# Performance work log

Measured on AMD Instinct MI355X. Metric: run time of the kernel, lower is better.

The kernel has to match this reference:

```python
import jax, jax.numpy as jnp
import numpy as np

B, C, H, W = 16, 64, 128, 128


def setup_inputs() -> dict:
    key = jax.random.key(0)
    k1, k2, k3 = jax.random.split(key, 3)
    return {
        "template_map": jax.random.normal(k1, (B, C, H, W), dtype=jnp.float32),
        "roi_map": jax.random.normal(k2, (B, C, H, W), dtype=jnp.float32),
        "gamma": jnp.zeros((1,), dtype=jnp.float32),
        "omega": jnp.zeros((1,), dtype=jnp.float32),
        "conv_w": jax.random.normal(k3, (C, 2 * C), dtype=jnp.float32) * 0.05,
        "conv_b": jnp.zeros((C,), dtype=jnp.float32),
    }


def _chan_attn(x):
    # x: [B, C, H, W] -> attention over channels [B, C, C] and flat values [B, C, N]
    b, c, h, w = x.shape
    v = x.reshape(b, c, h * w)
    energy = jnp.einsum('bcn,bdn->bcd', v, v)  # [B, C, C]
    energy_new = jnp.max(energy, axis=-1, keepdims=True) - energy
    attn = jax.nn.softmax(energy_new, axis=-1)
    return attn, v


def reference(template_map, roi_map, gamma, omega, conv_w, conv_b):
    b, c, th, tw = template_map.shape
    _, _, rh, rw = roi_map.shape
    t_attn, t_v = _chan_attn(template_map)
    r_attn, r_v = _chan_attn(roi_map)
    # cross application: roi attention reweights template channels, and vice versa
    t_out = jnp.einsum('bcd,bdn->bcn', r_attn, t_v).reshape(b, c, th, tw)
    t_out = gamma * t_out + template_map
    r_out = jnp.einsum('bcd,bdn->bcn', t_attn, r_v).reshape(b, c, rh, rw)
    r_out = omega * r_out + roi_map
    fused = jnp.concatenate([t_out, r_out], axis=1)  # [B, 2C, H, W]
    # 1x1 conv == channel-mixing einsum
    out = jnp.einsum('bchw,oc->bohw', fused, conv_w) + conv_b[None, :, None, None]
    return out
```

## Files before the change

### kernel.cpp

```cpp
#include <hip/hip_runtime.h>

typedef __attribute__((ext_vector_type(8))) short short8;
typedef __attribute__((ext_vector_type(4))) float floatx4;
typedef unsigned int uint;
typedef unsigned short ushort;

#define BATCH 16
#define CH 64
#define NPIX 16384
#define TWOC 128

__device__ __forceinline__ ushort f2bf(float f) {
    uint u = __float_as_uint(f);
    u += 0x7FFFu + ((u >> 16) & 1u);
    return (ushort)(u >> 16);
}

__global__ __launch_bounds__(256) void gram_kernel(
    const float* __restrict__ tmap, const float* __restrict__ rmap,
    const float* __restrict__ gamma, const float* __restrict__ omega,
    float* __restrict__ G)
{
    const int map = blockIdx.y;
    const float mult = (map == 0) ? omega[0] : gamma[0];
    if (mult == 0.f) return;

    __shared__ float tile[64][68];
    const int chunk = blockIdx.x;
    const int b     = blockIdx.z;
    const float* x = (map == 0 ? tmap : rmap) + (size_t)b * CH * NPIX + chunk * 512;
    const int t  = threadIdx.x;
    const int ti = t >> 4;
    const int tj = t & 15;

    float acc[4][4];
#pragma unroll
    for (int i = 0; i < 4; ++i)
#pragma unroll
        for (int j = 0; j < 4; ++j) acc[i][j] = 0.f;

    for (int tt = 0; tt < 8; ++tt) {
        const int col0 = tt * 64;
#pragma unroll
        for (int k = 0; k < 16; ++k) {
            int e = t + 256 * k;
            int c = e >> 6, col = e & 63;
            tile[c][col] = x[(size_t)c * NPIX + col0 + col];
        }
        __syncthreads();
#pragma unroll 8
        for (int n = 0; n < 64; n += 2) {
            float2 av[4], bv[4];
#pragma unroll
            for (int i = 0; i < 4; ++i) av[i] = *(const float2*)&tile[ti + 16 * i][n];
#pragma unroll
            for (int j = 0; j < 4; ++j) bv[j] = *(const float2*)&tile[tj + 16 * j][n];
#pragma unroll
            for (int i = 0; i < 4; ++i)
#pragma unroll
                for (int j = 0; j < 4; ++j) {
                    acc[i][j] += av[i].x * bv[j].x;
                    acc[i][j] += av[i].y * bv[j].y;
                }
        }
        __syncthreads();
    }
    float* Gp = G + ((size_t)(b * 2 + map) << 12);
#pragma unroll
    for (int i = 0; i < 4; ++i)
#pragma unroll
        for (int j = 0; j < 4; ++j)
            atomicAdd(&Gp[(ti + 16 * i) * 64 + (tj + 16 * j)], acc[i][j]);
}

__global__ __launch_bounds__(128) void finalize_kernel(
    const float* __restrict__ G, const float* __restrict__ gamma,
    const float* __restrict__ omega, const float* __restrict__ conv_w,
    ushort* __restrict__ Mtf)
{
    __shared__ float attn[2][64][64];
    const int b = blockIdx.x;
    const int t = threadIdx.x;
    const float gam = gamma[0], om = omega[0];
    {
        const int map = t >> 6, i = t & 63;
        const float need = (map == 0) ? om : gam;
        if (need != 0.f) {
            const float* Grow = G + ((size_t)(b * 2 + map) << 12) + i * 64;
            float mn = Grow[0];
            for (int j = 1; j < 64; ++j) mn = fminf(mn, Grow[j]);
            float s = 0.f;
            for (int j = 0; j < 64; ++j) s += expf(mn - Grow[j]);
            const float inv = 1.f / s;
            for (int j = 0; j < 64; ++j) attn[map][i][j] = expf(mn - Grow[j]) * inv;
        }
    }
    __syncthreads();
    for (int idx = t; idx < 8192; idx += 128) {
        const int e     = idx & 7;
        const int l     = (idx >> 3) & 63;
        const int mi    = (idx >> 9) & 3;
        const int kstep = idx >> 11;
        const int row = mi * 16 + (l & 15);
        const int k   = kstep * 32 + (l >> 4) * 8 + e;
        const float* wrow = conv_w + row * TWOC;
        float v = wrow[k];
        if (k < 64) {
            if (gam != 0.f) {
                float dot = 0.f;
                for (int c = 0; c < 64; ++c) dot += wrow[c] * attn[1][c][k];
                v += gam * dot;
            }
        } else {
            const int d = k - 64;
            if (om != 0.f) {
                float dot = 0.f;
                for (int c = 0; c < 64; ++c) dot += wrow[64 + c] * attn[0][c][d];
                v += om * dot;
            }
        }
        Mtf[(size_t)b * 8192 + idx] = f2bf(v);
    }
}

__global__ __launch_bounds__(256, 3) void out_kernel(
    const float* __restrict__ tmap, const float* __restrict__ rmap,
    const ushort* __restrict__ Mtf, const float* __restrict__ conv_b,
    float* __restrict__ out)
{
    const int b   = blockIdx.y;
    const int t   = threadIdx.x;
    const int w   = t >> 6;
    const int l   = t & 63;
    const int lg  = l >> 4;
    const int lj  = l & 15;
    const int pxw = blockIdx.x * 256 + w * 64;

    const ushort* mbase = Mtf + (size_t)b * 8192;

    floatx4 acc[4][4];
#pragma unroll
    for (int mi = 0; mi < 4; ++mi)
#pragma unroll
        for (int nj = 0; nj < 4; ++nj) acc[mi][nj] = (floatx4){0.f, 0.f, 0.f, 0.f};

#pragma unroll
    for (int h = 0; h < 2; ++h) {
        const float* src = ((h == 0) ? tmap : rmap) + (size_t)b * CH * NPIX;
#pragma unroll
        for (int ks = 0; ks < 2; ++ks) {
            short8 a[4];
#pragma unroll
            for (int mi = 0; mi < 4; ++mi)
                a[mi] = *(const short8*)&mbase[((((h * 2 + ks) * 4 + mi) * 64) + l) * 8];

#pragma unroll
            for (int nj = 0; nj < 4; ++nj) {
                const float* cbase = src + (size_t)(ks * 32 + lg * 8) * NPIX
                                         + pxw + nj * 16 + lj;
                float v[8];
#pragma unroll
                for (int e = 0; e < 8; ++e) v[e] = cbase[(size_t)e * NPIX];
                short8 bb;
#pragma unroll
                for (int e = 0; e < 8; ++e) bb[e] = (short)f2bf(v[e]);
#pragma unroll
                for (int mi = 0; mi < 4; ++mi)
                    acc[mi][nj] = __builtin_amdgcn_mfma_f32_16x16x32_bf16(
                        a[mi], bb, acc[mi][nj], 0, 0, 0);
            }
        }
    }

#pragma unroll
    for (int mi = 0; mi < 4; ++mi) {
#pragma unroll
        for (int r = 0; r < 4; ++r) {
            const int och = mi * 16 + lg * 4 + r;
            const float bv = conv_b[och];
            float* orow = out + ((size_t)b * CH + och) * NPIX;
#pragma unroll
            for (int nj = 0; nj < 4; ++nj)
                orow[pxw + nj * 16 + lj] = acc[mi][nj][r] + bv;
        }
    }
}

extern "C" void kernel_launch(void* const* d_in, const int* in_sizes, int n_in,
                              void* d_out, int out_size, void* d_ws, size_t ws_size,
                              hipStream_t stream) {
    const float* tmap   = (const float*)d_in[0];
    const float* rmap   = (const float*)d_in[1];
    const float* gamma  = (const float*)d_in[2];
    const float* omega  = (const float*)d_in[3];
    const float* conv_w = (const float*)d_in[4];
    const float* conv_b = (const float*)d_in[5];
    float* out = (float*)d_out;

    float*  G   = (float*)d_ws;
    ushort* Mtf = (ushort*)((char*)d_ws + (size_t)BATCH * 2 * 4096 * sizeof(float));

    hipMemsetAsync(d_ws, 0, (size_t)BATCH * 2 * 4096 * sizeof(float), stream);

    gram_kernel<<<dim3(32, 2, BATCH), 256, 0, stream>>>(tmap, rmap, gamma, omega, G);
    finalize_kernel<<<dim3(BATCH), 128, 0, stream>>>(G, gamma, omega, conv_w, Mtf);
    out_kernel<<<dim3(64, BATCH), 256, 0, stream>>>(tmap, rmap, Mtf, conv_b, out);
}
```

Measured before the change: 53.52 us.

## Stage bf16 input tiles and weight matrix in LDS for out_kernel MFMA

out_kernel now copies the per-batch bf16 mixing matrix into shared memory and loads input channels as float4 vectors. Pairs of channels are packed to bf16 and written to a padded LDS tile, and the MFMA B operands are then gathered from that tile. This replaces the scalar strided global loads, one float per channel per lane, with wide coalesced loads. In exchange it adds LDS traffic and two barriers per chunk, and the occupancy hint rises from 3 to 4 blocks.

New measurement: 54.46 us. Within noise of the previous version (+1.8%).

```diff
diff --git a/kernel.cpp b/kernel.cpp
--- a/kernel.cpp
+++ b/kernel.cpp
@@ -9,11 +9,15 @@
 #define CH 64
 #define NPIX 16384
 #define TWOC 128
+#define XSTR 260
 
 __device__ __forceinline__ ushort f2bf(float f) {
     uint u = __float_as_uint(f);
     u += 0x7FFFu + ((u >> 16) & 1u);
     return (ushort)(u >> 16);
+}
+__device__ __forceinline__ uint pk2(float lo, float hi) {
+    return (uint)f2bf(lo) | ((uint)f2bf(hi) << 16);
 }
 
 __global__ __launch_bounds__(256) void gram_kernel(
@@ -123,20 +127,28 @@
     }
 }
 
-__global__ __launch_bounds__(256, 3) void out_kernel(
+__global__ __launch_bounds__(256, 4) void out_kernel(
     const float* __restrict__ tmap, const float* __restrict__ rmap,
     const ushort* __restrict__ Mtf, const float* __restrict__ conv_b,
     float* __restrict__ out)
 {
+    __shared__ __align__(16) ushort Ms[8192];
+    __shared__ __align__(16) uint   Xs[16 * XSTR];
+
     const int b   = blockIdx.y;
     const int t   = threadIdx.x;
     const int w   = t >> 6;
     const int l   = t & 63;
     const int lg  = l >> 4;
     const int lj  = l & 15;
-    const int pxw = blockIdx.x * 256 + w * 64;
-
-    const ushort* mbase = Mtf + (size_t)b * 8192;
+    const int px0 = blockIdx.x * 256;
+
+    {
+        const uint4* src = (const uint4*)(Mtf + (size_t)b * 8192);
+        uint4* dst = (uint4*)Ms;
+#pragma unroll
+        for (int i = 0; i < 4; ++i) dst[t + 256 * i] = src[t + 256 * i];
+    }
 
     floatx4 acc[4][4];
 #pragma unroll
@@ -144,34 +156,56 @@
 #pragma unroll
         for (int nj = 0; nj < 4; ++nj) acc[mi][nj] = (floatx4){0.f, 0.f, 0.f, 0.f};
 
-#pragma unroll
-    for (int h = 0; h < 2; ++h) {
-        const float* src = ((h == 0) ? tmap : rmap) + (size_t)b * CH * NPIX;
-#pragma unroll
-        for (int ks = 0; ks < 2; ++ks) {
-            short8 a[4];
+    const float* tb = tmap + (size_t)b * CH * NPIX + px0;
+    const float* rb = rmap + (size_t)b * CH * NPIX + px0;
+
+#pragma unroll
+    for (int c = 0; c < 4; ++c) {
+        const float* src = ((c < 2) ? tb : rb) + (size_t)((c & 1) * 32) * NPIX;
+
+        float4 r0[4], r1[4];
+#pragma unroll
+        for (int it = 0; it < 4; ++it) {
+            const int p = it * 4 + w;
+            r0[it] = *(const float4*)&src[(size_t)(2 * p) * NPIX + 4 * l];
+            r1[it] = *(const float4*)&src[(size_t)(2 * p + 1) * NPIX + 4 * l];
+        }
+        __syncthreads();
+
+#pragma unroll
+        for (int it = 0; it < 4; ++it) {
+            const int p = it * 4 + w;
+            uint4 o;
+            o.x = pk2(r0[it].x, r1[it].x);
+            o.y = pk2(r0[it].y, r1[it].y);
+            o.z = pk2(r0[it].z, r1[it].z);
+            o.w = pk2(r0[it].w, r1[it].w);
+            *(uint4*)&Xs[p * XSTR + 4 * l] = o;
+        }
+        __syncthreads();
+
+        short8 a[4];
+#pragma unroll
+        for (int mi = 0; mi < 4; ++mi)
+            a[mi] = *(const short8*)&Ms[((c * 4 + mi) * 64 + l) * 8];
+
+#pragma unroll
+        for (int nj = 0; nj < 4; ++nj) {
+            const int pxl = w * 64 + nj * 16 + lj;
+            uint4 bu;
+            bu.x = Xs[(4 * lg + 0) * XSTR + pxl];
+            bu.y = Xs[(4 * lg + 1) * XSTR + pxl];
+            bu.z = Xs[(4 * lg + 2) * XSTR + pxl];
+            bu.w = Xs[(4 * lg + 3) * XSTR + pxl];
+            const short8 bb = *(const short8*)&bu;
 #pragma unroll
             for (int mi = 0; mi < 4; ++mi)
-                a[mi] = *(const short8*)&mbase[((((h * 2 + ks) * 4 + mi) * 64) + l) * 8];
-
-#pragma unroll
-            for (int nj = 0; nj < 4; ++nj) {
-                const float* cbase = src + (size_t)(ks * 32 + lg * 8) * NPIX
-                                         + pxw + nj * 16 + lj;
-                float v[8];
-#pragma unroll
-                for (int e = 0; e < 8; ++e) v[e] = cbase[(size_t)e * NPIX];
-                short8 bb;
-#pragma unroll
-                for (int e = 0; e < 8; ++e) bb[e] = (short)f2bf(v[e]);
-#pragma unroll
-                for (int mi = 0; mi < 4; ++mi)
-                    acc[mi][nj] = __builtin_amdgcn_mfma_f32_16x16x32_bf16(
-                        a[mi], bb, acc[mi][nj], 0, 0, 0);
-            }
-        }
-    }
-
+                acc[mi][nj] = __builtin_amdgcn_mfma_f32_16x16x32_bf16(
+                    a[mi], bb, acc[mi][nj], 0, 0, 0);
+        }
+    }
+
+    const int pxw = px0 + w * 64;
 #pragma unroll
     for (int mi = 0; mi < 4; ++mi) {
 #pragma unroll
```

## Stage out_kernel inputs via global_load_lds and vectorize output stores through LDS

Applied to the files above, without the earlier changes.

out_kernel now loads each 32-channel x 256-pixel slab into shared memory with 16-byte direct global-to-LDS loads. Previously each lane issued strided scalar 4-byte loads. Results are staged back through LDS so the output is written with 16-byte vector stores instead of scalar ones, and the occupancy hint rises from 3 to 4 blocks per SIMD. The cost is 32 KB of LDS per block, extra barriers with no double buffering, and possible LDS bank conflicts on the transposed reads.

Result: slower. 68.53 us (+28.0%).

```diff
diff --git a/kernel.cpp b/kernel.cpp
--- a/kernel.cpp
+++ b/kernel.cpp
@@ -14,6 +14,15 @@
     uint u = __float_as_uint(f);
     u += 0x7FFFu + ((u >> 16) & 1u);
     return (ushort)(u >> 16);
+}
+__device__ __forceinline__ uint pk2(float lo, float hi) {
+    return (uint)f2bf(lo) | ((uint)f2bf(hi) << 16);
+}
+
+typedef const __attribute__((address_space(1))) void gas_void;
+typedef __attribute__((address_space(3))) void las_void;
+__device__ __forceinline__ void gload16(const void* g, void* l) {
+    __builtin_amdgcn_global_load_lds((gas_void*)g, (las_void*)l, 16, 0, 0);
 }
 
 __global__ __launch_bounds__(256) void gram_kernel(
@@ -123,20 +132,24 @@
     }
 }
 
-__global__ __launch_bounds__(256, 3) void out_kernel(
+__global__ __launch_bounds__(256, 4) void out_kernel(
     const float* __restrict__ tmap, const float* __restrict__ rmap,
     const ushort* __restrict__ Mtf, const float* __restrict__ conv_b,
     float* __restrict__ out)
 {
+    __shared__ __align__(16) uint Xs[32 * 256];
+
     const int b   = blockIdx.y;
     const int t   = threadIdx.x;
     const int w   = t >> 6;
     const int l   = t & 63;
     const int lg  = l >> 4;
     const int lj  = l & 15;
-    const int pxw = blockIdx.x * 256 + w * 64;
+    const int px0 = blockIdx.x * 256;
 
     const ushort* mbase = Mtf + (size_t)b * 8192;
+    const float*  tb = tmap + (size_t)b * CH * NPIX + px0;
+    const float*  rb = rmap + (size_t)b * CH * NPIX + px0;
 
     floatx4 acc[4][4];
 #pragma unroll
@@ -145,44 +158,68 @@
         for (int nj = 0; nj < 4; ++nj) acc[mi][nj] = (floatx4){0.f, 0.f, 0.f, 0.f};
 
 #pragma unroll
-    for (int h = 0; h < 2; ++h) {
-        const float* src = ((h == 0) ? tmap : rmap) + (size_t)b * CH * NPIX;
-#pragma unroll
-        for (int ks = 0; ks < 2; ++ks) {
-            short8 a[4];
+    for (int c = 0; c < 4; ++c) {
+        const float* src = ((c < 2) ? tb : rb) + (size_t)((c & 1) * 32) * NPIX;
+
+#pragma unroll
+        for (int i = 0; i < 8; ++i) {
+            const int row = i * 4 + w;
+            gload16(src + (size_t)row * NPIX + 4 * l, &Xs[row * 256]);
+        }
+
+        short8 a[4];
+#pragma unroll
+        for (int mi = 0; mi < 4; ++mi)
+            a[mi] = *(const short8*)&mbase[((c * 4 + mi) * 64 + l) * 8];
+
+        __syncthreads();
+
+#pragma unroll
+        for (int nj = 0; nj < 4; ++nj) {
+            const int pxl = w * 64 + nj * 16 + lj;
+            float v[8];
+#pragma unroll
+            for (int e = 0; e < 8; ++e)
+                v[e] = __uint_as_float(Xs[(8 * lg + e) * 256 + pxl]);
+            uint4 bu;
+            bu.x = pk2(v[0], v[1]);
+            bu.y = pk2(v[2], v[3]);
+            bu.z = pk2(v[4], v[5]);
+            bu.w = pk2(v[6], v[7]);
+            const short8 bb = *(const short8*)&bu;
 #pragma unroll
             for (int mi = 0; mi < 4; ++mi)
-                a[mi] = *(const short8*)&mbase[((((h * 2 + ks) * 4 + mi) * 64) + l) * 8];
-
-#pragma unroll
-            for (int nj = 0; nj < 4; ++nj) {
-                const float* cbase = src + (size_t)(ks * 32 + lg * 8) * NPIX
-                                         + pxw + nj * 16 + lj;
-                float v[8];
-#pragma unroll
-                for (int e = 0; e < 8; ++e) v[e] = cbase[(size_t)e * NPIX];
-                short8 bb;
-#pragma unroll
-                for (int e = 0; e < 8; ++e) bb[e] = (short)f2bf(v[e]);
-#pragma unroll
-                for (int mi = 0; mi < 4; ++mi)
-                    acc[mi][nj] = __builtin_amdgcn_mfma_f32_16x16x32_bf16(
-                        a[mi], bb, acc[mi][nj], 0, 0, 0);
+                acc[mi][nj] = __builtin_amdgcn_mfma_f32_16x16x32_bf16(
+                    a[mi], bb, acc[mi][nj], 0, 0, 0);
+        }
+        __syncthreads();
+    }
+
+    uint* buf = Xs;
+#pragma unroll
+    for (int pass = 0; pass < 2; ++pass) {
+#pragma unroll
+        for (int gh = 0; gh < 2; ++gh) {
+            const int g = pass * 2 + gh;
+#pragma unroll
+            for (int nj = 0; nj < 4; ++nj)
+#pragma unroll
+                for (int r = 0; r < 4; ++r)
+                    buf[(gh * 16 + lg * 4 + r) * 256 + w * 64 + nj * 16 + lj] =
+                        __float_as_uint(acc[g][nj][r] + conv_b[g * 16 + lg * 4 + r]);
+        }
+        __syncthreads();
+#pragma unroll
+        for (int gh = 0; gh < 2; ++gh) {
+            const int g = pass * 2 + gh;
+#pragma unroll
+            for (int j = 0; j < 4; ++j) {
+                const int ol = w + 4 * j;
+                const uint4 val = *(const uint4*)&buf[(gh * 16 + ol) * 256 + 4 * l];
+                *(uint4*)&out[((size_t)b * CH + g * 16 + ol) * NPIX + px0 + 4 * l] = val;
             }
         }
-    }
-
-#pragma unroll
-    for (int mi = 0; mi < 4; ++mi) {
-#pragma unroll
-        for (int r = 0; r < 4; ++r) {
-            const int och = mi * 16 + lg * 4 + r;
-            const float bv = conv_b[och];
-            float* orow = out + ((size_t)b * CH + och) * NPIX;
-#pragma unroll
-            for (int nj = 0; nj < 4; ++nj)
-                orow[pxw + nj * 16 + lj] = acc[mi][nj][r] + bv;
-        }
+        if (pass == 0) __syncthreads();
     }
 }
 
```
